# Kernel optimization log

Measured on AMD Instinct MI355X. Metric: run time of the kernel, lower is better.

The kernel has to match this reference:

```python
import jax, jax.numpy as jnp
import numpy as np

EPS = 1e-12   # F.normalize default eps
TH = 0.5      # forward-arg default threshold
CLAMP_LO, CLAMP_HI = 0.01, 0.999


def setup_inputs() -> dict:
    key = jax.random.key(0)
    k1, k2 = jax.random.split(key)
    # x4: ResNet layer3 features after ala1 scaling + upfeat, stride-16 of a 1024px image
    x4 = jax.random.normal(k1, (8, 1024, 64, 64), dtype=jnp.float32)
    # logits: classifier output after upfeat, same spatial grid, 21 classes
    logits = jax.random.normal(k2, (8, 21, 64, 64), dtype=jnp.float32)
    return {"x4": x4, "logits": logits, "pcm": 2}


def reference(x4, logits, pcm):
    b, c, h, w = x4.shape
    hw = h * w
    xf = x4.reshape(b, c, hw)                      # [b, c, hw]
    # F.normalize(dim=1): x / max(||x||_2, eps)
    norm = jnp.sqrt(jnp.sum(xf * xf, axis=1, keepdims=True))
    xn = xf / jnp.maximum(norm, EPS)
    # pixel affinity: [b, hw, hw]
    aff = jnp.einsum('bci,bcj->bij', xn, xn)
    aff = jnp.clip(aff, CLAMP_LO, CLAMP_HI)
    aff = jnp.where(aff < TH, jnp.zeros((), aff.dtype), aff)
    # column-normalize (torch sum over dim=1)
    aff = aff / jnp.sum(aff, axis=1, keepdims=True)
    lf = logits.reshape(b, -1, hw)                 # [b, K, hw]
    for _ in range(pcm):                           # pcm is a Python int
        lf = jnp.einsum('bki,bij->bkj', lf, aff)
    return lf.reshape(b, -1, h, w)
```

## Files before the change

### kernel.cpp

```cpp
#include <hip/hip_runtime.h>
#include <hip/hip_bf16.h>

#define B_  8
#define C_  1024
#define HW_ 4096
#define NK  21
#define NT  32
#define NTRI (NT * (NT + 1) / 2)

using bf16 = __hip_bfloat16;
typedef __attribute__((ext_vector_type(4))) float float4_;

__global__ __launch_bounds__(256) void knorm1(const float* __restrict__ x4, float* __restrict__ sumsq) {
    int t = threadIdx.x;
    int b = blockIdx.z;
    int c0 = blockIdx.y * 128;
    int j = blockIdx.x * 256 + t;
    const float* p = x4 + ((size_t)b * C_ + c0) * HW_ + j;
    float s = 0.f;
#pragma unroll 8
    for (int c = 0; c < 128; ++c) {
        float v = p[(size_t)c * HW_];
        s = fmaf(v, v, s);
    }
    atomicAdd(&sumsq[b * HW_ + j], s);
}

__global__ __launch_bounds__(256) void ktrans(const float* __restrict__ x4, const float* __restrict__ sumsq,
                                              unsigned char* __restrict__ Xn8) {
    int b = blockIdx.z, ct = blockIdx.y, jt = blockIdx.x;
    int c0 = ct * 64, j0 = jt * 64;
    int t = threadIdx.x;
    __shared__ float tile[64][65];

    int jl = t & 63, cl = t >> 6;
#pragma unroll
    for (int cc = 0; cc < 16; ++cc) {
        int c = cc * 4 + cl;
        tile[c][jl] = x4[((size_t)b * C_ + c0 + c) * HW_ + j0 + jl];
    }
    __syncthreads();

    int j = t >> 2, cb = (t & 3) * 16;
    int jg = j0 + j;
    float inv = 1.0f / fmaxf(sqrtf(sumsq[b * HW_ + jg]), 1e-12f);

    unsigned int pk[4];
#pragma unroll
    for (int q = 0; q < 4; ++q) {
        float f0 = tile[cb + q * 4 + 0][j] * inv;
        float f1 = tile[cb + q * 4 + 1][j] * inv;
        float f2 = tile[cb + q * 4 + 2][j] * inv;
        float f3 = tile[cb + q * 4 + 3][j] * inv;
        unsigned int r = 0;
        r = __builtin_amdgcn_cvt_pk_fp8_f32(f0, f1, r, false);
        r = __builtin_amdgcn_cvt_pk_fp8_f32(f2, f3, r, true);
        pk[q] = r;
    }
    uint4 v = make_uint4(pk[0], pk[1], pk[2], pk[3]);
    *(uint4*)(Xn8 + ((size_t)b * HW_ + jg) * C_ + c0 + cb) = v;
}

__global__ __launch_bounds__(256) void kgram(const unsigned char* __restrict__ Xn8, bf16* __restrict__ aff,
                                             float* __restrict__ colsum, int* __restrict__ flags) {
    int b = blockIdx.y;
    int p = blockIdx.x;
    int it = (int)((2.0f * NT + 1.0f - sqrtf((2.0f * NT + 1.0f) * (2.0f * NT + 1.0f) - 8.0f * (float)p)) * 0.5f);
    while (it > 0 && p < it * NT - it * (it - 1) / 2) --it;
    while (p >= (it + 1) * NT - (it + 1) * it / 2) ++it;
    int jt = it + p - (it * NT - it * (it - 1) / 2);

    int i0 = it * 128, j0 = jt * 128;
    int t = threadIdx.x, w = t >> 6, l = t & 63;
    int wr = w >> 1, wc = w & 1;
    int lrow = l & 15, lk = l >> 4;

    __shared__ __align__(16) unsigned char As[128 * 128];
    __shared__ __align__(16) unsigned char Bs[128 * 128];
    __shared__ int fl;

    const unsigned char* XA = Xn8 + ((size_t)b * HW_ + i0) * C_;
    const unsigned char* XB = Xn8 + ((size_t)b * HW_ + j0) * C_;

    int srow = l >> 3;
    int sslot = l & 7;

    float4_ acc[4][4];
#pragma unroll
    for (int m = 0; m < 4; ++m)
#pragma unroll
        for (int n = 0; n < 4; ++n) acc[m][n] = {0.f, 0.f, 0.f, 0.f};

    int swz = (lrow >> 1) & 7;

    for (int k0 = 0; k0 < C_; k0 += 128) {
        __syncthreads();
#pragma unroll
        for (int q = 0; q < 4; ++q) {
            int R = (w * 4 + q) * 8 + srow;
            int gp = sslot ^ ((R >> 1) & 7);
            __builtin_amdgcn_global_load_lds(
                (const __attribute__((address_space(1))) void*)(XA + (size_t)R * C_ + k0 + gp * 16),
                (__attribute__((address_space(3))) void*)(As + R * 128 + sslot * 16), 16, 0, 0);
            __builtin_amdgcn_global_load_lds(
                (const __attribute__((address_space(1))) void*)(XB + (size_t)R * C_ + k0 + gp * 16),
                (__attribute__((address_space(3))) void*)(Bs + R * 128 + sslot * 16), 16, 0, 0);
        }
        __syncthreads();
#pragma unroll
        for (int ks = 0; ks < 4; ++ks) {
            int cc = ks * 4 + lk;
            int off = ((cc >> 1) ^ swz) * 16 + (cc & 1) * 8;
            long av[4], bv[4];
#pragma unroll
            for (int m = 0; m < 4; ++m) {
                int r = wr * 64 + m * 16 + lrow;
                av[m] = *(const long*)(As + r * 128 + off);
            }
#pragma unroll
            for (int n = 0; n < 4; ++n) {
                int r = wc * 64 + n * 16 + lrow;
                bv[n] = *(const long*)(Bs + r * 128 + off);
            }
#pragma unroll
            for (int m = 0; m < 4; ++m)
#pragma unroll
                for (int n = 0; n < 4; ++n)
                    acc[m][n] = __builtin_amdgcn_mfma_f32_16x16x32_fp8_fp8(av[m], bv[n], acc[m][n], 0, 0, 0);
        }
    }

    bool any = false;
#pragma unroll
    for (int m = 0; m < 4; ++m)
#pragma unroll
        for (int n = 0; n < 4; ++n)
#pragma unroll
            for (int r = 0; r < 4; ++r) any |= (acc[m][n][r] >= 0.5f);

    if (t == 0) fl = 0;
    __syncthreads();
    unsigned long long bal = __ballot(any);
    if (l == 0 && bal != 0ull) atomicOr(&fl, 1);
    __syncthreads();
    bool mirror = (it != jt);
    if (t == 0) {
        flags[(b * NT + it) * NT + jt] = fl;
        if (mirror) flags[(b * NT + jt) * NT + it] = fl;
    }

    if (fl) {
        size_t affb = (size_t)b * HW_ * HW_;
        float rsum[4][4];
#pragma unroll
        for (int m = 0; m < 4; ++m)
#pragma unroll
            for (int r = 0; r < 4; ++r) rsum[m][r] = 0.f;

#pragma unroll
        for (int n = 0; n < 4; ++n) {
            int j = j0 + wc * 64 + n * 16 + lrow;
            float cs = 0.f;
#pragma unroll
            for (int m = 0; m < 4; ++m) {
#pragma unroll
                for (int r = 0; r < 4; ++r) {
                    float v = acc[m][n][r];
                    v = fminf(fmaxf(v, 0.01f), 0.999f);
                    v = (v < 0.5f) ? 0.0f : v;
                    bf16 bb = __float2bfloat16(v);
                    int i = i0 + wr * 64 + m * 16 + lk * 4 + r;
                    aff[affb + (size_t)i * HW_ + j] = bb;
                    float bf = __bfloat162float(bb);
                    cs += bf;
                    rsum[m][r] += bf;
                    if (mirror) aff[affb + (size_t)j * HW_ + i] = bb;
                }
            }
            cs += __shfl_xor(cs, 16);
            cs += __shfl_xor(cs, 32);
            if (lk == 0) atomicAdd(&colsum[b * HW_ + j], cs);
        }
        if (mirror) {
#pragma unroll
            for (int m = 0; m < 4; ++m) {
#pragma unroll
                for (int r = 0; r < 4; ++r) {
                    float s = rsum[m][r];
                    s += __shfl_xor(s, 1);
                    s += __shfl_xor(s, 2);
                    s += __shfl_xor(s, 4);
                    s += __shfl_xor(s, 8);
                    if (lrow == 0) {
                        int i = i0 + wr * 64 + m * 16 + lk * 4 + r;
                        atomicAdd(&colsum[b * HW_ + i], s);
                    }
                }
            }
        }
    }
}

__global__ __launch_bounds__(128) void kprop(const float* __restrict__ lf, const bf16* __restrict__ aff,
                                             const int* __restrict__ flags, const float* __restrict__ colsum,
                                             float* __restrict__ outp) {
    int b = blockIdx.y, jt = blockIdx.x;
    int t = threadIdx.x;
    int j = jt * 128 + t;
    __shared__ float lfs[NK * 128];
    float acc[NK];
#pragma unroll
    for (int k = 0; k < NK; ++k) acc[k] = 0.f;

    for (int it = 0; it < NT; ++it) {
        if (flags[(b * NT + it) * NT + jt] == 0) continue;
        __syncthreads();
        for (int idx = t; idx < NK * 128; idx += 128)
            lfs[idx] = lf[((size_t)b * NK + (idx >> 7)) * HW_ + it * 128 + (idx & 127)];
        __syncthreads();
        const bf16* ap = aff + ((size_t)b * HW_ + it * 128) * HW_ + j;
        for (int ii = 0; ii < 128; ++ii) {
            float a = __bfloat162float(ap[(size_t)ii * HW_]);
#pragma unroll
            for (int k = 0; k < NK; ++k)
                acc[k] = fmaf(lfs[(k << 7) + ii], a, acc[k]);
        }
    }
    float inv = 1.0f / colsum[b * HW_ + j];
#pragma unroll
    for (int k = 0; k < NK; ++k)
        outp[((size_t)b * NK + k) * HW_ + j] = acc[k] * inv;
}

extern "C" void kernel_launch(void* const* d_in, const int* in_sizes, int n_in,
                              void* d_out, int out_size, void* d_ws, size_t ws_size,
                              hipStream_t stream) {
    const float* x4 = (const float*)d_in[0];
    const float* logits = (const float*)d_in[1];
    float* out = (float*)d_out;

    char* w = (char*)d_ws;
    size_t off = 0;
    auto take = [&](size_t bytes) {
        char* p = w + off;
        off += (bytes + 255) & ~(size_t)255;
        return p;
    };
    unsigned char* Xn8 = (unsigned char*)take((size_t)B_ * HW_ * C_);
    bf16* aff     = (bf16*)take((size_t)B_ * HW_ * HW_ * 2);
    float* colsum = (float*)take((size_t)B_ * HW_ * 4);
    int*   flags  = (int*)take((size_t)B_ * NT * NT * 4);
    float* sumsq  = (float*)take((size_t)B_ * HW_ * 4);
    float* lf1    = (float*)take((size_t)B_ * NK * HW_ * 4);

    hipMemsetAsync(colsum, 0, (size_t)B_ * HW_ * 4 + (size_t)B_ * NT * NT * 4 + (size_t)B_ * HW_ * 4, stream);

    knorm1<<<dim3(HW_ / 256, 8, B_), dim3(256), 0, stream>>>(x4, sumsq);
    ktrans<<<dim3(HW_ / 64, C_ / 64, B_), dim3(256), 0, stream>>>(x4, sumsq, Xn8);
    kgram <<<dim3(NTRI, B_), dim3(256), 0, stream>>>(Xn8, aff, colsum, flags);

    kprop<<<dim3(NT, B_), dim3(128), 0, stream>>>(logits, aff, flags, colsum, lf1);
    kprop<<<dim3(NT, B_), dim3(128), 0, stream>>>(lf1, aff, flags, colsum, out);
}
```

Before: 395.4 us.

## Permute fp8 K layout so gram kernel loads 16-byte LDS fragments

The transpose kernel now writes normalized fp8 features in a permuted channel order within each 128-channel block, so each lane's two consecutive MFMA k-steps sit in one contiguous 16-byte chunk. The gram kernel then reads 128-bit LDS vectors instead of 64-bit ones, halving LDS read instructions, and uses a simpler row-based XOR swizzle. Since the dot product is order-invariant, permuting K consistently for A and B keeps results the same. ktrans also switches to 128-channel tiles with a larger shared tile, which may affect occupancy.

Result: faster. 367.7 us (-7.0%).

```diff
diff --git a/kernel.cpp b/kernel.cpp
--- a/kernel.cpp
+++ b/kernel.cpp
@@ -10,6 +10,7 @@
 
 using bf16 = __hip_bfloat16;
 typedef __attribute__((ext_vector_type(4))) float float4_;
+typedef __attribute__((ext_vector_type(2))) long long2_;
 
 __global__ __launch_bounds__(256) void knorm1(const float* __restrict__ x4, float* __restrict__ sumsq) {
     int t = threadIdx.x;
@@ -29,36 +30,43 @@
 __global__ __launch_bounds__(256) void ktrans(const float* __restrict__ x4, const float* __restrict__ sumsq,
                                               unsigned char* __restrict__ Xn8) {
     int b = blockIdx.z, ct = blockIdx.y, jt = blockIdx.x;
-    int c0 = ct * 64, j0 = jt * 64;
+    int c0 = ct * 128, j0 = jt * 64;
     int t = threadIdx.x;
-    __shared__ float tile[64][65];
+    __shared__ float tile[128][65];
 
     int jl = t & 63, cl = t >> 6;
 #pragma unroll
-    for (int cc = 0; cc < 16; ++cc) {
-        int c = cc * 4 + cl;
-        tile[c][jl] = x4[((size_t)b * C_ + c0 + c) * HW_ + j0 + jl];
-    }
+    for (int cc = 0; cc < 128; cc += 4)
+        tile[cc + cl][jl] = x4[((size_t)b * C_ + c0 + cc + cl) * HW_ + j0 + jl];
     __syncthreads();
 
-    int j = t >> 2, cb = (t & 3) * 16;
+    int j = t >> 2, q = t & 3;
     int jg = j0 + j;
     float inv = 1.0f / fmaxf(sqrtf(sumsq[b * HW_ + jg]), 1e-12f);
 
-    unsigned int pk[4];
-#pragma unroll
-    for (int q = 0; q < 4; ++q) {
-        float f0 = tile[cb + q * 4 + 0][j] * inv;
-        float f1 = tile[cb + q * 4 + 1][j] * inv;
-        float f2 = tile[cb + q * 4 + 2][j] * inv;
-        float f3 = tile[cb + q * 4 + 3][j] * inv;
-        unsigned int r = 0;
-        r = __builtin_amdgcn_cvt_pk_fp8_f32(f0, f1, r, false);
-        r = __builtin_amdgcn_cvt_pk_fp8_f32(f2, f3, r, true);
-        pk[q] = r;
-    }
-    uint4 v = make_uint4(pk[0], pk[1], pk[2], pk[3]);
-    *(uint4*)(Xn8 + ((size_t)b * HW_ + jg) * C_ + c0 + cb) = v;
+#pragma unroll
+    for (int pass = 0; pass < 2; ++pass) {
+        int u = pass * 4 + q;
+        int p = u >> 2, lk = u & 3;
+        unsigned int pk[4];
+#pragma unroll
+        for (int h = 0; h < 2; ++h) {
+            int kbase = (2 * p + h) * 32 + lk * 8;
+#pragma unroll
+            for (int g = 0; g < 2; ++g) {
+                float f0 = tile[kbase + g * 4 + 0][j] * inv;
+                float f1 = tile[kbase + g * 4 + 1][j] * inv;
+                float f2 = tile[kbase + g * 4 + 2][j] * inv;
+                float f3 = tile[kbase + g * 4 + 3][j] * inv;
+                unsigned int r = 0;
+                r = __builtin_amdgcn_cvt_pk_fp8_f32(f0, f1, r, false);
+                r = __builtin_amdgcn_cvt_pk_fp8_f32(f2, f3, r, true);
+                pk[h * 2 + g] = r;
+            }
+        }
+        *(uint4*)(Xn8 + ((size_t)b * HW_ + jg) * C_ + c0 + u * 16) =
+            make_uint4(pk[0], pk[1], pk[2], pk[3]);
+    }
 }
 
 __global__ __launch_bounds__(256) void kgram(const unsigned char* __restrict__ Xn8, bf16* __restrict__ aff,
@@ -91,14 +99,12 @@
 #pragma unroll
         for (int n = 0; n < 4; ++n) acc[m][n] = {0.f, 0.f, 0.f, 0.f};
 
-    int swz = (lrow >> 1) & 7;
-
     for (int k0 = 0; k0 < C_; k0 += 128) {
         __syncthreads();
 #pragma unroll
         for (int q = 0; q < 4; ++q) {
             int R = (w * 4 + q) * 8 + srow;
-            int gp = sslot ^ ((R >> 1) & 7);
+            int gp = sslot ^ (R & 7);
             __builtin_amdgcn_global_load_lds(
                 (const __attribute__((address_space(1))) void*)(XA + (size_t)R * C_ + k0 + gp * 16),
                 (__attribute__((address_space(3))) void*)(As + R * 128 + sslot * 16), 16, 0, 0);
@@ -108,25 +114,25 @@
         }
         __syncthreads();
 #pragma unroll
-        for (int ks = 0; ks < 4; ++ks) {
-            int cc = ks * 4 + lk;
-            int off = ((cc >> 1) ^ swz) * 16 + (cc & 1) * 8;
-            long av[4], bv[4];
+        for (int pp = 0; pp < 2; ++pp) {
+            long2_ av[4], bv[4];
 #pragma unroll
             for (int m = 0; m < 4; ++m) {
                 int r = wr * 64 + m * 16 + lrow;
-                av[m] = *(const long*)(As + r * 128 + off);
+                av[m] = *(const long2_*)(As + r * 128 + ((pp * 4 + lk) ^ (r & 7)) * 16);
             }
 #pragma unroll
             for (int n = 0; n < 4; ++n) {
                 int r = wc * 64 + n * 16 + lrow;
-                bv[n] = *(const long*)(Bs + r * 128 + off);
+                bv[n] = *(const long2_*)(Bs + r * 128 + ((pp * 4 + lk) ^ (r & 7)) * 16);
             }
 #pragma unroll
             for (int m = 0; m < 4; ++m)
 #pragma unroll
-                for (int n = 0; n < 4; ++n)
-                    acc[m][n] = __builtin_amdgcn_mfma_f32_16x16x32_fp8_fp8(av[m], bv[n], acc[m][n], 0, 0, 0);
+                for (int n = 0; n < 4; ++n) {
+                    acc[m][n] = __builtin_amdgcn_mfma_f32_16x16x32_fp8_fp8(av[m].x, bv[n].x, acc[m][n], 0, 0, 0);
+                    acc[m][n] = __builtin_amdgcn_mfma_f32_16x16x32_fp8_fp8(av[m].y, bv[n].y, acc[m][n], 0, 0, 0);
+                }
         }
     }
 
@@ -256,7 +262,7 @@
     hipMemsetAsync(colsum, 0, (size_t)B_ * HW_ * 4 + (size_t)B_ * NT * NT * 4 + (size_t)B_ * HW_ * 4, stream);
 
     knorm1<<<dim3(HW_ / 256, 8, B_), dim3(256), 0, stream>>>(x4, sumsq);
-    ktrans<<<dim3(HW_ / 64, C_ / 64, B_), dim3(256), 0, stream>>>(x4, sumsq, Xn8);
+    ktrans<<<dim3(HW_ / 64, C_ / 128, B_), dim3(256), 0, stream>>>(x4, sumsq, Xn8);
     kgram <<<dim3(NTRI, B_), dim3(256), 0, stream>>>(Xn8, aff, colsum, flags);
 
     kprop<<<dim3(NT, B_), dim3(128), 0, stream>>>(logits, aff, flags, colsum, lf1);
```
